# Kernel tuning notes

Hardware: AMD Instinct MI355X
Metric: run time of the kernel (lower is better)

Reference implementation:

```python
import jax, jax.numpy as jnp
import numpy as np

NUM_ITER = 64
M_CONST = jnp.array([-1.0, 1.0], dtype=jnp.float32)      # constellation m
ALPHA   = jnp.array([0.5, 0.5], dtype=jnp.float32)       # prior alpha


def setup_inputs() -> dict:
    key = jax.random.key(0)
    k1, k2, k3 = jax.random.split(key, 3)
    B, N_RX, N_TX = 16384, 64, 32
    # channel matrix, scaled ~1/sqrt(N_rx) like a normalized MIMO channel
    Ht = jax.random.normal(k1, (B, N_RX, N_TX), dtype=jnp.float32) / jnp.sqrt(jnp.float32(N_RX))
    yt = jax.random.normal(k2, (B, N_RX), dtype=jnp.float32)
    sigmat0 = jax.random.uniform(k3, (B,), dtype=jnp.float32, minval=0.1, maxval=0.6)
    taui = jnp.ones((NUM_ITER + 1,), dtype=jnp.float32)          # taui0 = 1
    delta = jnp.full((NUM_ITER,), 0.01, dtype=jnp.float32)       # small step size for stability
    return {"yt": yt, "Ht": Ht, "sigmat0": sigmat0, "taui": taui, "delta": delta}


def _cmdnet(yt, Ht, sigmat0, taui, delta):
    m = M_CONST                      # [M]
    log_alpha = jnp.log(ALPHA)       # [M]
    sig2 = (sigmat0 ** 2)[:, None, None]          # [B,1,1]
    B, _, K = Ht.shape
    M = m.shape[0]

    # G0 = zeros broadcast to [B, K, M]
    G = jnp.zeros((B, K, M), dtype=Ht.dtype)
    tau = jnp.abs(taui[0])
    ft = jax.nn.softmax((log_alpha + G) * tau, axis=-1)   # [B,K,M]
    xt = jnp.sum(ft * m, axis=-1)                         # [B,K]

    HH = jnp.einsum('bnk,bnl->bkl', Ht, Ht)               # [B,K,K]
    yH = jnp.einsum('bn,bnk->bk', yt, Ht)                 # [B,K]

    def step(carry, xs):
        G, ft, xt, tau = carry
        d_i, tau_next = xs
        xHH = jnp.einsum('bk,bkl->bl', xt, HH)            # [B,K]
        grad_x = tau * (ft * m - ft * xt[..., None])      # [B,K,M]
        grad_L = sig2 * (1.0 - jnp.exp(-G)) + grad_x * (xHH - yH)[..., None]
        G = G - d_i * grad_L
        tau = jnp.abs(tau_next)
        ft = jax.nn.softmax((log_alpha + G) * tau, axis=-1)
        xt = jnp.sum(ft * m, axis=-1)
        return (G, ft, xt, tau), None

    (G, ft, xt, tau), _ = jax.lax.scan(step, (G, ft, xt, tau), (delta, taui[1:]))
    return ft, xt


def reference(yt, Ht, sigmat0, taui, delta):
    return _cmdnet(yt, Ht, sigmat0, taui, delta)
```

## Files before the change

### kernel.cpp

```cpp
#include <hip/hip_runtime.h>


#define NRX 64
#define KSYM 32

typedef float  f32x16 __attribute__((ext_vector_type(16)));
typedef short  short8 __attribute__((ext_vector_type(8)));
typedef _Float16 h16x2 __attribute__((ext_vector_type(2)));

__device__ __forceinline__ float readlane_f(float v, int lane) {
    return __int_as_float(__builtin_amdgcn_readlane(__float_as_int(v), lane));
}
__device__ __forceinline__ unsigned cvt_pk_bf16(float a, float b) {
    unsigned r;
    asm("v_cvt_pk_bf16_f32 %0, %1, %2" : "=v"(r) : "v"(a), "v"(b));
    return r;
}
__device__ __forceinline__ int cvt_pk_f16(float a, float b) {
    int r;
    asm("v_cvt_pkrtz_f16_f32 %0, %1, %2" : "=v"(r) : "v"(a), "v"(b));
    return r;
}
#define DPP_ROR(DST, SRC, J)                                                   \
    asm("v_mov_b32_dpp %0, %1 row_ror:" #J " row_mask:0xf bank_mask:0xf"       \
        : "=v"(DST) : "v"(SRC))

__device__ __forceinline__ float dot2_f16(int a, int b, float c) {
#if __has_builtin(__builtin_amdgcn_fdot2)
    union { int i; h16x2 h; } ua, ub;
    ua.i = a; ub.i = b;
    return __builtin_amdgcn_fdot2(ua.h, ub.h, c, false);
#else
    float r = c;
    asm("v_dot2_f32_f16 %0, %1, %2, %0" : "+v"(r) : "v"(a), "v"(b));
    return r;
#endif
}
__device__ __forceinline__ float exp2_fast(float x) {
#if __has_builtin(__builtin_amdgcn_exp2f)
    return __builtin_amdgcn_exp2f(x);
#else
    float r; asm("v_exp_f32 %0, %1" : "=v"(r) : "v"(x)); return r;
#endif
}
__device__ __forceinline__ float xor16_f(float x) {
#if __has_builtin(__builtin_amdgcn_permlane16_swap)
    typedef unsigned uint2v __attribute__((ext_vector_type(2)));
    unsigned xi = __float_as_int(x);
    uint2v pr = __builtin_amdgcn_permlane16_swap(xi, xi, false, false);
    return (__uint_as_float(pr[0]) + __uint_as_float(pr[1])) - x;
#else
    return __int_as_float(
        __builtin_amdgcn_ds_swizzle(__float_as_int(x), 0x401F));
#endif
}

union FragU { unsigned u[4]; short8 s; };

__global__ __launch_bounds__(256, 4) void cmdnet_kernel(
    const float* __restrict__ yt,
    const float* __restrict__ Ht,
    const float* __restrict__ sigmat0,
    const float* __restrict__ taui,
    const float* __restrict__ delta,
    float* __restrict__ out_ft,
    float* __restrict__ out_xt,
    int niter)
{
    __shared__ __align__(16) float hhbuf[4][2][KSYM * KSYM];
    __shared__ __align__(16) float ytL[4][2][NRX];

    const int tid  = threadIdx.x;
    const int w    = tid >> 6;
    const int lane = tid & 63;
    const int k    = lane & 31;
    const int h    = lane >> 5;
    const int hi8  = h * 8;
    const int bb   = blockIdx.x * 8 + w * 2;
    const int b    = bb + h;
    const float LOG2E = 1.4426950408889634f;

    ytL[w][0][lane] = yt[(size_t)bb * NRX + lane];
    ytL[w][1][lane] = yt[(size_t)bb * NRX + NRX + lane];

    float dreg = 0.f, treg = 1.f;
    if (lane < niter) { dreg = delta[lane] * LOG2E; treg = fabsf(taui[lane + 1]); }

    float sig2 = sigmat0[b];
    sig2 *= sig2;

    float yhp0 = 0.f, yhp1 = 0.f;

    #pragma unroll
    for (int s = 0; s < 2; ++s) {
        f32x16 acc;
        #pragma unroll
        for (int j = 0; j < 16; ++j) acc[j] = 0.f;

        const float* Hb = Ht + ((size_t)(bb + s)) * (NRX * KSYM);
        #pragma unroll
        for (int c = 0; c < 4; ++c) {
            const float* base = Hb + (c * 16 + hi8) * KSYM + k;
            float f[8];
            #pragma unroll
            for (int e = 0; e < 8; ++e) f[e] = base[e * KSYM];

            float4 ya = *reinterpret_cast<const float4*>(&ytL[w][s][c * 16 + hi8]);
            float4 yb = *reinterpret_cast<const float4*>(&ytL[w][s][c * 16 + hi8 + 4]);
            float yp = (s == 0) ? yhp0 : yhp1;
            yp = fmaf(ya.x, f[0], yp); yp = fmaf(ya.y, f[1], yp);
            yp = fmaf(ya.z, f[2], yp); yp = fmaf(ya.w, f[3], yp);
            yp = fmaf(yb.x, f[4], yp); yp = fmaf(yb.y, f[5], yp);
            yp = fmaf(yb.z, f[6], yp); yp = fmaf(yb.w, f[7], yp);
            if (s == 0) yhp0 = yp; else yhp1 = yp;

            FragU hiF, loF;
            #pragma unroll
            for (int p = 0; p < 4; ++p) {
                unsigned hp = cvt_pk_bf16(f[2*p], f[2*p+1]);
                float h0 = __uint_as_float(hp << 16);
                float h1 = __uint_as_float(hp & 0xffff0000u);
                loF.u[p] = cvt_pk_bf16(f[2*p] - h0, f[2*p+1] - h1);
                hiF.u[p] = hp;
            }
            acc = __builtin_amdgcn_mfma_f32_32x32x16_bf16(hiF.s, hiF.s, acc, 0, 0, 0);
            acc = __builtin_amdgcn_mfma_f32_32x32x16_bf16(hiF.s, loF.s, acc, 0, 0, 0);
            acc = __builtin_amdgcn_mfma_f32_32x32x16_bf16(loF.s, hiF.s, acc, 0, 0, 0);
        }

        float* buf_s = &hhbuf[w][s][0];
        #pragma unroll
        for (int j = 0; j < 16; ++j) {
            int row = (j & 3) + 8 * (j >> 2) + 4 * h;
            buf_s[row * 32 + k] = acc[j];
        }
    }

    int own_pk[16];
    {
        const int low4 = k & 15;
        const float* rowp = &hhbuf[w][h][k * 32];
        own_pk[0] = cvt_pk_f16(0.5f * rowp[k], 0.5f * rowp[k ^ 16]);
        #define GATH(J) { \
            int idx; DPP_ROR(idx, low4, J); \
            own_pk[J] = cvt_pk_f16(0.5f * rowp[(k & 16) | idx], \
                                   0.5f * rowp[((k & 16) ^ 16) | idx]); }
        GATH(1)  GATH(2)  GATH(3)  GATH(4)  GATH(5)
        GATH(6)  GATH(7)  GATH(8)  GATH(9)  GATH(10)
        GATH(11) GATH(12) GATH(13) GATH(14) GATH(15)
        #undef GATH
    }

    float yh0 = yhp0 + __shfl_xor(yhp0, 32, 64);
    float yh1 = yhp1 + __shfl_xor(yhp1, 32, 64);
    float yh  = 0.5f * (h ? yh1 : yh0);

    float tau = fabsf(taui[0]);
    float Gl0 = 0.f, Gl1 = 0.f;
    float xt = 0.f;

    for (int i = 0; i < niter; ++i) {
        float d2       = readlane_f(dreg, i);
        float tau_next = readlane_f(treg, i);

        float e0 = exp2_fast(-Gl0);
        float e1 = exp2_fast(-Gl1);

        float xts = xor16_f(xt);
        int xpk = cvt_pk_f16(xt, xts);

        float a0 = -yh, a1 = 0.f, a2 = 0.f, a3 = 0.f;
        a0 = dot2_f16(own_pk[0], xpk, a0);
        #define STEP(J) {                                                      \
            int xr; DPP_ROR(xr, xpk, J);                                       \
            float& aa = ((J) & 3) == 0 ? a0 : ((J) & 3) == 1 ? a1              \
                       : ((J) & 3) == 2 ? a2 : a3;                             \
            aa = dot2_f16(own_pk[J], xr, aa); }
        STEP(1)  STEP(2)  STEP(3)  STEP(4)  STEP(5)
        STEP(6)  STEP(7)  STEP(8)  STEP(9)  STEP(10)
        STEP(11) STEP(12) STEP(13) STEP(14) STEP(15)
        #undef STEP
        float r = (a0 + a1) + (a2 + a3);

        float t  = fmaf(-xt, xt, 1.0f);
        float p  = tau * t * r;
        float g0 = fmaf(sig2, 1.f - e0, -p);
        float g1 = fmaf(sig2, 1.f - e1,  p);
        Gl0 = fmaf(-d2, g0, Gl0);
        Gl1 = fmaf(-d2, g1, Gl1);

        tau = tau_next;
        float z2 = tau * (Gl1 - Gl0);
        float ez = exp2_fast(-fabsf(z2));
        float sg = __builtin_amdgcn_rcpf(1.f + ez);
        float m  = (1.f - ez) * sg;
        xt = __builtin_copysignf(m, z2);
    }

    float ft1 = fmaf(0.5f, xt, 0.5f);
    float ft0 = 1.f - ft1;
    float2 f2 = make_float2(ft0, ft1);
    reinterpret_cast<float2*>(out_ft)[(size_t)b * KSYM + k] = f2;
    out_xt[(size_t)b * KSYM + k] = xt;
}

extern "C" void kernel_launch(void* const* d_in, const int* in_sizes, int n_in,
                              void* d_out, int out_size, void* d_ws, size_t ws_size,
                              hipStream_t stream) {
    const float* yt    = (const float*)d_in[0];
    const float* Ht    = (const float*)d_in[1];
    const float* sg    = (const float*)d_in[2];
    const float* taui  = (const float*)d_in[3];
    const float* delta = (const float*)d_in[4];
    int B     = in_sizes[2];
    int niter = in_sizes[4];
    float* out    = (float*)d_out;
    float* out_ft = out;
    float* out_xt = out + (size_t)B * 64;

    dim3 grid(B / 8), block(256);
    hipLaunchKernelGGL(cmdnet_kernel, grid, block, 0, stream,
                       yt, Ht, sg, taui, delta, out_ft, out_xt, niter);
}
```

Baseline: 77.30 us.

## Split kernel into Gram prep pass and high-occupancy iteration pass

Splits the fused kernel in two. The first kernel computes the packed f16 Gram rows and yH per symbol and writes them to workspace. The second kernel reloads them without LDS at a higher launch-bounds occupancy (8 blocks) so the serial 64-iteration loop hides more latency. In exchange it adds an extra launch and a workspace round-trip of about 34 MB, and falls back to the monolithic kernel when workspace is too small.

```diff
diff --git a/kernel.cpp b/kernel.cpp
--- a/kernel.cpp
+++ b/kernel.cpp
@@ -57,38 +57,14 @@
 
 union FragU { unsigned u[4]; short8 s; };
 
-__global__ __launch_bounds__(256, 4) void cmdnet_kernel(
-    const float* __restrict__ yt,
-    const float* __restrict__ Ht,
-    const float* __restrict__ sigmat0,
-    const float* __restrict__ taui,
-    const float* __restrict__ delta,
-    float* __restrict__ out_ft,
-    float* __restrict__ out_xt,
-    int niter)
-{
-    __shared__ __align__(16) float hhbuf[4][2][KSYM * KSYM];
-    __shared__ __align__(16) float ytL[4][2][NRX];
-
-    const int tid  = threadIdx.x;
-    const int w    = tid >> 6;
-    const int lane = tid & 63;
-    const int k    = lane & 31;
-    const int h    = lane >> 5;
-    const int hi8  = h * 8;
-    const int bb   = blockIdx.x * 8 + w * 2;
-    const int b    = bb + h;
-    const float LOG2E = 1.4426950408889634f;
-
-    ytL[w][0][lane] = yt[(size_t)bb * NRX + lane];
-    ytL[w][1][lane] = yt[(size_t)bb * NRX + NRX + lane];
-
-    float dreg = 0.f, treg = 1.f;
-    if (lane < niter) { dreg = delta[lane] * LOG2E; treg = fabsf(taui[lane + 1]); }
-
-    float sig2 = sigmat0[b];
-    sig2 *= sig2;
-
+
+__device__ __forceinline__ void compute_ownpk_yh(
+    const float* __restrict__ Ht, float* hh_w, const float* yt_w,
+    int bb, int lane, int own_pk[16], float& yh_out)
+{
+    const int k   = lane & 31;
+    const int h   = lane >> 5;
+    const int hi8 = h * 8;
     float yhp0 = 0.f, yhp1 = 0.f;
 
     #pragma unroll
@@ -105,8 +81,8 @@
             #pragma unroll
             for (int e = 0; e < 8; ++e) f[e] = base[e * KSYM];
 
-            float4 ya = *reinterpret_cast<const float4*>(&ytL[w][s][c * 16 + hi8]);
-            float4 yb = *reinterpret_cast<const float4*>(&ytL[w][s][c * 16 + hi8 + 4]);
+            float4 ya = *reinterpret_cast<const float4*>(&yt_w[s * NRX + c * 16 + hi8]);
+            float4 yb = *reinterpret_cast<const float4*>(&yt_w[s * NRX + c * 16 + hi8 + 4]);
             float yp = (s == 0) ? yhp0 : yhp1;
             yp = fmaf(ya.x, f[0], yp); yp = fmaf(ya.y, f[1], yp);
             yp = fmaf(ya.z, f[2], yp); yp = fmaf(ya.w, f[3], yp);
@@ -127,8 +103,7 @@
             acc = __builtin_amdgcn_mfma_f32_32x32x16_bf16(hiF.s, loF.s, acc, 0, 0, 0);
             acc = __builtin_amdgcn_mfma_f32_32x32x16_bf16(loF.s, hiF.s, acc, 0, 0, 0);
         }
-
-        float* buf_s = &hhbuf[w][s][0];
+        float* buf_s = hh_w + s * (KSYM * KSYM);
         #pragma unroll
         for (int j = 0; j < 16; ++j) {
             int row = (j & 3) + 8 * (j >> 2) + 4 * h;
@@ -136,10 +111,9 @@
         }
     }
 
-    int own_pk[16];
     {
         const int low4 = k & 15;
-        const float* rowp = &hhbuf[w][h][k * 32];
+        const float* rowp = hh_w + h * (KSYM * KSYM) + k * 32;
         own_pk[0] = cvt_pk_f16(0.5f * rowp[k], 0.5f * rowp[k ^ 16]);
         #define GATH(J) { \
             int idx; DPP_ROR(idx, low4, J); \
@@ -153,9 +127,14 @@
 
     float yh0 = yhp0 + __shfl_xor(yhp0, 32, 64);
     float yh1 = yhp1 + __shfl_xor(yhp1, 32, 64);
-    float yh  = 0.5f * (h ? yh1 : yh0);
-
-    float tau = fabsf(taui[0]);
+    yh_out = 0.5f * (h ? yh1 : yh0);
+}
+
+__device__ __forceinline__ float run_iters(
+    const int own_pk[16], float yh, float sig2, float tau0,
+    float dreg, float treg, int niter)
+{
+    float tau = tau0;
     float Gl0 = 0.f, Gl1 = 0.f;
     float xt = 0.f;
 
@@ -196,11 +175,106 @@
         float m  = (1.f - ez) * sg;
         xt = __builtin_copysignf(m, z2);
     }
+    return xt;
+}
+
+__global__ __launch_bounds__(256, 4) void cmdnet_prep(
+    const float* __restrict__ yt, const float* __restrict__ Ht,
+    int* __restrict__ ws_pk,
+    float* __restrict__ ws_yh)
+{
+    __shared__ __align__(16) float hhbuf[4][2][KSYM * KSYM];
+    __shared__ __align__(16) float ytL[4][2][NRX];
+
+    const int tid  = threadIdx.x;
+    const int w    = tid >> 6;
+    const int lane = tid & 63;
+    const int k    = lane & 31;
+    const int h    = lane >> 5;
+    const int bb   = blockIdx.x * 8 + w * 2;
+    const int b    = bb + h;
+
+    ytL[w][0][lane] = yt[(size_t)bb * NRX + lane];
+    ytL[w][1][lane] = yt[(size_t)bb * NRX + NRX + lane];
+
+    int own_pk[16]; float yh;
+    compute_ownpk_yh(Ht, &hhbuf[w][0][0], &ytL[w][0][0], bb, lane, own_pk, yh);
+
+    int* dst = ws_pk + ((size_t)b * 32 + k) * 16;
+    #pragma unroll
+    for (int q = 0; q < 4; ++q)
+        reinterpret_cast<int4*>(dst)[q] =
+            make_int4(own_pk[4*q], own_pk[4*q+1], own_pk[4*q+2], own_pk[4*q+3]);
+    ws_yh[(size_t)b * 32 + k] = yh;
+}
+
+__global__ __launch_bounds__(256, 8) void cmdnet_loop(
+    const int* __restrict__ ws_pk, const float* __restrict__ ws_yh,
+    const float* __restrict__ sigmat0,
+    const float* __restrict__ taui, const float* __restrict__ delta,
+    float* __restrict__ out_ft, float* __restrict__ out_xt, int niter)
+{
+    const int tid  = threadIdx.x;
+    const int w    = tid >> 6;
+    const int lane = tid & 63;
+    const int k    = lane & 31;
+    const int h    = lane >> 5;
+    const int b    = blockIdx.x * 8 + w * 2 + h;
+    const float LOG2E = 1.4426950408889634f;
+
+    float dreg = 0.f, treg = 1.f;
+    if (lane < niter) { dreg = delta[lane] * LOG2E; treg = fabsf(taui[lane + 1]); }
+
+    int own_pk[16];
+    const int* src = ws_pk + ((size_t)b * 32 + k) * 16;
+    #pragma unroll
+    for (int q = 0; q < 4; ++q) {
+        int4 v = reinterpret_cast<const int4*>(src)[q];
+        own_pk[4*q] = v.x; own_pk[4*q+1] = v.y; own_pk[4*q+2] = v.z; own_pk[4*q+3] = v.w;
+    }
+    float yh = ws_yh[(size_t)b * 32 + k];
+    float sig2 = sigmat0[b]; sig2 *= sig2;
+
+    float xt = run_iters(own_pk, yh, sig2, fabsf(taui[0]), dreg, treg, niter);
 
     float ft1 = fmaf(0.5f, xt, 0.5f);
-    float ft0 = 1.f - ft1;
-    float2 f2 = make_float2(ft0, ft1);
-    reinterpret_cast<float2*>(out_ft)[(size_t)b * KSYM + k] = f2;
+    reinterpret_cast<float2*>(out_ft)[(size_t)b * KSYM + k] = make_float2(1.f - ft1, ft1);
+    out_xt[(size_t)b * KSYM + k] = xt;
+}
+
+__global__ __launch_bounds__(256, 4) void cmdnet_mono(
+    const float* __restrict__ yt, const float* __restrict__ Ht,
+    const float* __restrict__ sigmat0,
+    const float* __restrict__ taui, const float* __restrict__ delta,
+    float* __restrict__ out_ft, float* __restrict__ out_xt, int niter)
+{
+    __shared__ __align__(16) float hhbuf[4][2][KSYM * KSYM];
+    __shared__ __align__(16) float ytL[4][2][NRX];
+
+    const int tid  = threadIdx.x;
+    const int w    = tid >> 6;
+    const int lane = tid & 63;
+    const int k    = lane & 31;
+    const int h    = lane >> 5;
+    const int bb   = blockIdx.x * 8 + w * 2;
+    const int b    = bb + h;
+    const float LOG2E = 1.4426950408889634f;
+
+    ytL[w][0][lane] = yt[(size_t)bb * NRX + lane];
+    ytL[w][1][lane] = yt[(size_t)bb * NRX + NRX + lane];
+
+    float dreg = 0.f, treg = 1.f;
+    if (lane < niter) { dreg = delta[lane] * LOG2E; treg = fabsf(taui[lane + 1]); }
+
+    float sig2 = sigmat0[b]; sig2 *= sig2;
+
+    int own_pk[16]; float yh;
+    compute_ownpk_yh(Ht, &hhbuf[w][0][0], &ytL[w][0][0], bb, lane, own_pk, yh);
+
+    float xt = run_iters(own_pk, yh, sig2, fabsf(taui[0]), dreg, treg, niter);
+
+    float ft1 = fmaf(0.5f, xt, 0.5f);
+    reinterpret_cast<float2*>(out_ft)[(size_t)b * KSYM + k] = make_float2(1.f - ft1, ft1);
     out_xt[(size_t)b * KSYM + k] = xt;
 }
 
@@ -218,7 +292,16 @@
     float* out_ft = out;
     float* out_xt = out + (size_t)B * 64;
 
+    size_t need = (size_t)B * 32 * 16 * sizeof(int) + (size_t)B * 32 * sizeof(float);
     dim3 grid(B / 8), block(256);
-    hipLaunchKernelGGL(cmdnet_kernel, grid, block, 0, stream,
-                       yt, Ht, sg, taui, delta, out_ft, out_xt, niter);
-}
+    if (ws_size >= need) {
+        int*   ws_pk = (int*)d_ws;
+        float* ws_yh = (float*)((char*)d_ws + (size_t)B * 32 * 16 * sizeof(int));
+        hipLaunchKernelGGL(cmdnet_prep, grid, block, 0, stream, yt, Ht, ws_pk, ws_yh);
+        hipLaunchKernelGGL(cmdnet_loop, grid, block, 0, stream,
+                           ws_pk, ws_yh, sg, taui, delta, out_ft, out_xt, niter);
+    } else {
+        hipLaunchKernelGGL(cmdnet_mono, grid, block, 0, stream,
+                           yt, Ht, sg, taui, delta, out_ft, out_xt, niter);
+    }
+}
```

New measurement: 95.33 us. +23.3%, slower.
